# Optimization experiments

Measured on AMD Instinct MI355X. Metric: run time of the kernel, lower is better.

Reference implementation:

```python
import jax, jax.numpy as jnp
import numpy as np

VOCAB_SIZE = 126
N_LABELS = VOCAB_SIZE + 2  # 128
START_IDX = N_LABELS - 2
STOP_IDX = N_LABELS - 1
NEG_INF = -10000.0


def setup_inputs() -> dict:
    key = jax.random.key(0)
    k1, k2, k3 = jax.random.split(key, 3)
    B, T = 512, 512
    logits = jax.random.normal(k1, (B, T, N_LABELS), dtype=jnp.float32)
    lens = jax.random.randint(k2, (B,), 1, T + 1, dtype=jnp.int64)
    transitions = jax.random.normal(k3, (N_LABELS, N_LABELS), dtype=jnp.float32)
    # CRF constraints from __init__: nothing transitions FROM start-as-target row,
    # nothing transitions INTO stop column (transitions[i, j] = score j -> i).
    transitions = transitions.at[START_IDX, :].set(NEG_INF)
    transitions = transitions.at[:, STOP_IDX].set(NEG_INF)
    return {"logits": logits, "lens": lens, "transitions": transitions}


def reference(logits, lens, transitions):
    """CRF forward algorithm (log partition function). Returns [B] norm."""
    B, T, n = logits.shape
    alpha0 = jnp.full((B, n), NEG_INF, dtype=logits.dtype).at[:, START_IDX].set(0.0)
    # mask[t, b] = 1 while t < lens[b] (matches c_lens > 0 per-step update)
    mask = (jnp.arange(T)[:, None] < lens[None, :]).astype(logits.dtype)  # [T, B]
    logits_t = jnp.transpose(logits, (1, 0, 2))  # [T, B, n]

    def step(alpha, inp):
        logit, m = inp  # [B, n], [B]
        # alpha_nxt[b, i] = logit[b, i] + logsumexp_j(trans[i, j] + alpha[b, j])
        alpha_nxt = jax.nn.logsumexp(transitions[None, :, :] + alpha[:, None, :], axis=2) + logit
        m = m[:, None]
        alpha = m * alpha_nxt + (1.0 - m) * alpha
        return alpha, None

    alpha, _ = jax.lax.scan(step, alpha0, (logits_t, mask))
    alpha = alpha + transitions[STOP_IDX][None, :]
    return jax.nn.logsumexp(alpha, axis=1)  # [B]
```

## Files before the change

### kernel.cpp

```cpp
#include <hip/hip_runtime.h>

#define NL 128
#define TT 512
#define NB 512
#define START_IDX 126
#define STOP_IDX 127

typedef __attribute__((ext_vector_type(8))) short bf16x8;
typedef __attribute__((ext_vector_type(4))) float f32x4;

__device__ __forceinline__ short f2bf(float x) {
    union { float f; unsigned u; } v; v.f = x;
    unsigned r = (v.u + 0x7FFFu + ((v.u >> 16) & 1u)) >> 16;
    return (short)r;
}

__global__ __launch_bounds__(256, 2)
void crf_fwd_kernel(const float* __restrict__ logits,
                    const int* __restrict__ lens,
                    const float* __restrict__ trans,
                    float* __restrict__ out)
{
    const int b    = blockIdx.x;
    const int tid  = threadIdx.x;
    const int wave = tid >> 6;
    const int lane = tid & 63;
    const int col  = lane & 15;
    const int kgrp = lane >> 4;

    __shared__ __align__(16) short Vbuf[2][NL];
    __shared__ float red[4];

    bf16x8 bfrag[2][4];
    #pragma unroll
    for (int n = 0; n < 2; ++n) {
        const int label = wave * 32 + n * 16 + col;
        #pragma unroll
        for (int kk = 0; kk < 4; ++kk) {
            const float* tp = trans + label * NL + kk * 32 + kgrp * 8;
            bf16x8 f;
            #pragma unroll
            for (int m = 0; m < 8; ++m) f[m] = f2bf(__expf(tp[m]));
            bfrag[n][kk] = f;
        }
    }
    const int lbl0 = wave * 32 + col;
    const int lbl1 = lbl0 + 16;
    const float ets0 = __expf(trans[STOP_IDX * NL + lbl0]);
    const float ets1 = __expf(trans[STOP_IDX * NL + lbl1]);

    int len = lens[b];
    len = len < 1 ? 1 : (len > TT ? TT : len);

    if (tid < NL) Vbuf[0][tid] = (tid == START_IDX) ? (short)0x3F80 : (short)0;

    const float* lg = logits + (size_t)b * (TT * NL);
    float l0 = lg[lbl0];
    float l1 = lg[lbl1];
    float c  = 0.f;
    float nv0 = 0.f, nv1 = 0.f;

    __syncthreads();

    for (int t = 0; t < len; ++t) {
        const short* vb = Vbuf[t & 1];
        const int tn = (t + 1 < len) ? t + 1 : t;
        const float pl0 = lg[tn * NL + lbl0];
        const float pl1 = lg[tn * NL + lbl1];

        f32x4 acc0 = {0.f, 0.f, 0.f, 0.f};
        f32x4 acc1 = {0.f, 0.f, 0.f, 0.f};
        #pragma unroll
        for (int kk = 0; kk < 4; ++kk) {
            bf16x8 af = *(const bf16x8*)(vb + kk * 32 + kgrp * 8);
            acc0 = __builtin_amdgcn_mfma_f32_16x16x32_bf16(af, bfrag[0][kk], acc0, 0, 0, 0);
            acc1 = __builtin_amdgcn_mfma_f32_16x16x32_bf16(af, bfrag[1][kk], acc1, 0, 0, 0);
        }

        nv0 = acc0[0] * __expf(l0);
        nv1 = acc1[0] * __expf(l1);

        if ((t & 3) == 3) {
            float m = fmaxf(nv0, nv1);
            m = fmaxf(m, __shfl_xor(m, 1));
            m = fmaxf(m, __shfl_xor(m, 2));
            m = fmaxf(m, __shfl_xor(m, 4));
            m = fmaxf(m, __shfl_xor(m, 8));
            if (lane == 0) red[wave] = m;
            __syncthreads();
            m = fmaxf(fmaxf(red[0], red[1]), fmaxf(red[2], red[3]));
            union { float f; unsigned u; } mu; mu.f = m;
            const int eb = (int)(mu.u >> 23);
            union { float f; unsigned u; } sc;
            sc.u = (unsigned)(253 - eb) << 23;
            nv0 *= sc.f; nv1 *= sc.f;
            c += (float)(eb - 126) * 0.69314718055994531f;
        }

        if (lane < 16) {
            short* vw = Vbuf[(t + 1) & 1];
            vw[lbl0] = f2bf(nv0);
            vw[lbl1] = f2bf(nv1);
        }
        l0 = pl0; l1 = pl1;
        __syncthreads();
    }

    float p = nv0 * ets0 + nv1 * ets1;
    p += __shfl_xor(p, 1);
    p += __shfl_xor(p, 2);
    p += __shfl_xor(p, 4);
    p += __shfl_xor(p, 8);
    if (lane == 0) red[wave] = p;
    __syncthreads();
    if (tid == 0) out[b] = c + __logf(red[0] + red[1] + red[2] + red[3]);
}

extern "C" void kernel_launch(void* const* d_in, const int* in_sizes, int n_in,
                              void* d_out, int out_size, void* d_ws, size_t ws_size,
                              hipStream_t stream) {
    const float* logits = (const float*)d_in[0];
    const int*   lens   = (const int*)d_in[1];
    const float* trans  = (const float*)d_in[2];
    float*       outp   = (float*)d_out;
    crf_fwd_kernel<<<NB, 256, 0, stream>>>(logits, lens, trans, outp);
}
```

Measured before the change: 187.7 us.

## Batch 16 sequences per wave with register-resident alpha and exp precompute

Replaces the one-block-per-sequence scan with a single-wave kernel that handles 16 sequences at once. The transposed problem puts exp(transitions) in MFMA A fragments and keeps alpha packed as bf16 in registers, so the per-step LDS round trip and block barriers go away. A separate pre-pass writes exp(logits) into workspace in a permuted order, with a fallback that computes exp inline. Renormalisation now runs every 8 steps, and logits are prefetched two steps ahead. The catch is that only 32 waves are launched, which leaves most of the GPU idle, and each wave iterates to the longest length among its 16 sequences.

```diff
diff --git a/kernel.cpp b/kernel.cpp
--- a/kernel.cpp
+++ b/kernel.cpp
@@ -8,6 +8,7 @@
 
 typedef __attribute__((ext_vector_type(8))) short bf16x8;
 typedef __attribute__((ext_vector_type(4))) float f32x4;
+typedef __attribute__((ext_vector_type(4))) unsigned u32x4;
 
 __device__ __forceinline__ short f2bf(float x) {
     union { float f; unsigned u; } v; v.f = x;
@@ -15,105 +16,165 @@
     return (short)r;
 }
 
-__global__ __launch_bounds__(256, 2)
-void crf_fwd_kernel(const float* __restrict__ logits,
-                    const int* __restrict__ lens,
-                    const float* __restrict__ trans,
-                    float* __restrict__ out)
+__device__ __forceinline__ unsigned cvt_pk_bf16(float lo, float hi) {
+    unsigned r;
+    asm("v_cvt_pk_bf16_f32 %0, %1, %2" : "=v"(r) : "v"(lo), "v"(hi));
+    return r;
+}
+
+__global__ __launch_bounds__(256)
+void exp_pre(const float* __restrict__ logits, const int* __restrict__ lens,
+             float* __restrict__ elp)
 {
-    const int b    = blockIdx.x;
-    const int tid  = threadIdx.x;
-    const int wave = tid >> 6;
-    const int lane = tid & 63;
-    const int col  = lane & 15;
-    const int kgrp = lane >> 4;
+    const int b = blockIdx.x;
+    int len = lens[b]; len = len < 1 ? 1 : (len > TT ? TT : len);
+    const float* src = logits + (size_t)b * TT * NL;
+    float*       dst = elp    + (size_t)b * TT * NL;
+    for (int idx = threadIdx.x; idx < len * 32; idx += 256) {
+        const int t = idx >> 5, q = idx & 31;
+        const int lbl = (q & 7) * 16 + (q >> 3) * 4;
+        f32x4 v = *(const f32x4*)(src + t * NL + lbl);
+        f32x4 e = { __expf(v[0]), __expf(v[1]), __expf(v[2]), __expf(v[3]) };
+        *(f32x4*)(dst + t * NL + q * 4) = e;
+    }
+}
 
-    __shared__ __align__(16) short Vbuf[2][NL];
-    __shared__ float red[4];
+#define LOADEL(E, T_) do {                                                    \
+    const float* _p = elsrc + lbase + (size_t)(T_) * NL;                      \
+    _Pragma("unroll")                                                         \
+    for (int m_ = 0; m_ < 8; ++m_) {                                          \
+        const int off_ = RAW ? (m_ * 16 + 4 * g) : (g * 32 + m_ * 4);         \
+        E[m_] = *(const f32x4*)(_p + off_);                                   \
+    }                                                                         \
+} while (0)
 
-    bf16x8 bfrag[2][4];
+#define STEP(T_, ECUR) do {                                                   \
+    f32x4 acc_[8];                                                            \
+    _Pragma("unroll") for (int m_ = 0; m_ < 8; ++m_)                          \
+        acc_[m_] = (f32x4){0.f, 0.f, 0.f, 0.f};                               \
+    _Pragma("unroll") for (int kk_ = 0; kk_ < 4; ++kk_) {                     \
+        u32x4 bu_ = { bw[kk_][0], bw[kk_][1], bw[kk_][2], bw[kk_][3] };       \
+        bf16x8 bv_ = __builtin_bit_cast(bf16x8, bu_);                         \
+        _Pragma("unroll") for (int m_ = 0; m_ < 8; ++m_)                      \
+            acc_[m_] = __builtin_amdgcn_mfma_f32_16x16x32_bf16(               \
+                afr[m_][kk_], bv_, acc_[m_], 0, 0, 0);                        \
+    }                                                                         \
+    const bool live_ = (T_) < len;                                            \
+    float nv_[8][4];                                                          \
+    _Pragma("unroll") for (int m_ = 0; m_ < 8; ++m_)                          \
+        _Pragma("unroll") for (int r_ = 0; r_ < 4; ++r_) {                    \
+            float el_ = ECUR[m_][r_];                                         \
+            if (RAW) el_ = __expf(el_);                                       \
+            nv_[m_][r_] = acc_[m_][r_] * el_;                                 \
+        }                                                                     \
+    { int tl_ = (T_) + 2; if (tl_ > TT - 1) tl_ = TT - 1; LOADEL(ECUR, tl_); }\
+    if ((((T_) & 7) == 7)) {                                                  \
+        float mx_ = nv_[0][0];                                                \
+        _Pragma("unroll") for (int m_ = 0; m_ < 8; ++m_)                      \
+            _Pragma("unroll") for (int r_ = 0; r_ < 4; ++r_)                  \
+                mx_ = fmaxf(mx_, nv_[m_][r_]);                                \
+        mx_ = fmaxf(mx_, __shfl_xor(mx_, 16));                                \
+        mx_ = fmaxf(mx_, __shfl_xor(mx_, 32));                                \
+        const unsigned eb_ = (__float_as_uint(mx_) >> 23) & 0xFFu;            \
+        const float sc_ = __uint_as_float(((253u - eb_) & 0xFFu) << 23);      \
+        _Pragma("unroll") for (int m_ = 0; m_ < 8; ++m_)                      \
+            _Pragma("unroll") for (int r_ = 0; r_ < 4; ++r_)                  \
+                nv_[m_][r_] *= sc_;                                           \
+        if (live_) cb += (float)((int)eb_ - 126) * 0.69314718055994531f;      \
+    }                                                                         \
+    _Pragma("unroll") for (int kk_ = 0; kk_ < 4; ++kk_) {                     \
+        const unsigned p0_ = cvt_pk_bf16(nv_[kk_][0],     nv_[kk_][1]);       \
+        const unsigned p1_ = cvt_pk_bf16(nv_[kk_][2],     nv_[kk_][3]);       \
+        const unsigned p2_ = cvt_pk_bf16(nv_[kk_ + 4][0], nv_[kk_ + 4][1]);   \
+        const unsigned p3_ = cvt_pk_bf16(nv_[kk_ + 4][2], nv_[kk_ + 4][3]);   \
+        if (live_) {                                                          \
+            bw[kk_][0] = p0_; bw[kk_][1] = p1_;                               \
+            bw[kk_][2] = p2_; bw[kk_][3] = p3_;                               \
+        }                                                                     \
+    }                                                                         \
+} while (0)
+
+template<bool RAW>
+__global__ __launch_bounds__(64)
+void crf_scan(const float* __restrict__ logits,
+              const int* __restrict__ lens,
+              const float* __restrict__ trans,
+              const float* __restrict__ elp,
+              float* __restrict__ out)
+{
+    const int b0   = blockIdx.x * 16;
+    const int lane = threadIdx.x;
+    const int c    = lane & 15;
+    const int g    = lane >> 4;
+
+    bf16x8 afr[8][4];
     #pragma unroll
-    for (int n = 0; n < 2; ++n) {
-        const int label = wave * 32 + n * 16 + col;
+    for (int m = 0; m < 8; ++m) {
+        const float* rowp = trans + (m * 16 + c) * NL + 4 * g;
         #pragma unroll
         for (int kk = 0; kk < 4; ++kk) {
-            const float* tp = trans + label * NL + kk * 32 + kgrp * 8;
-            bf16x8 f;
+            f32x4 lo4 = *(const f32x4*)(rowp + kk * 16);
+            f32x4 hi4 = *(const f32x4*)(rowp + (kk + 4) * 16);
+            bf16x8 a;
             #pragma unroll
-            for (int m = 0; m < 8; ++m) f[m] = f2bf(__expf(tp[m]));
-            bfrag[n][kk] = f;
+            for (int j = 0; j < 4; ++j) {
+                a[j]     = f2bf(__expf(lo4[j]));
+                a[j + 4] = f2bf(__expf(hi4[j]));
+            }
+            afr[m][kk] = a;
         }
     }
-    const int lbl0 = wave * 32 + col;
-    const int lbl1 = lbl0 + 16;
-    const float ets0 = __expf(trans[STOP_IDX * NL + lbl0]);
-    const float ets1 = __expf(trans[STOP_IDX * NL + lbl1]);
 
-    int len = lens[b];
-    len = len < 1 ? 1 : (len > TT ? TT : len);
-
-    if (tid < NL) Vbuf[0][tid] = (tid == START_IDX) ? (short)0x3F80 : (short)0;
-
-    const float* lg = logits + (size_t)b * (TT * NL);
-    float l0 = lg[lbl0];
-    float l1 = lg[lbl1];
-    float c  = 0.f;
-    float nv0 = 0.f, nv1 = 0.f;
-
-    __syncthreads();
-
-    for (int t = 0; t < len; ++t) {
-        const short* vb = Vbuf[t & 1];
-        const int tn = (t + 1 < len) ? t + 1 : t;
-        const float pl0 = lg[tn * NL + lbl0];
-        const float pl1 = lg[tn * NL + lbl1];
-
-        f32x4 acc0 = {0.f, 0.f, 0.f, 0.f};
-        f32x4 acc1 = {0.f, 0.f, 0.f, 0.f};
-        #pragma unroll
-        for (int kk = 0; kk < 4; ++kk) {
-            bf16x8 af = *(const bf16x8*)(vb + kk * 32 + kgrp * 8);
-            acc0 = __builtin_amdgcn_mfma_f32_16x16x32_bf16(af, bfrag[0][kk], acc0, 0, 0, 0);
-            acc1 = __builtin_amdgcn_mfma_f32_16x16x32_bf16(af, bfrag[1][kk], acc1, 0, 0, 0);
-        }
-
-        nv0 = acc0[0] * __expf(l0);
-        nv1 = acc1[0] * __expf(l1);
-
-        if ((t & 3) == 3) {
-            float m = fmaxf(nv0, nv1);
-            m = fmaxf(m, __shfl_xor(m, 1));
-            m = fmaxf(m, __shfl_xor(m, 2));
-            m = fmaxf(m, __shfl_xor(m, 4));
-            m = fmaxf(m, __shfl_xor(m, 8));
-            if (lane == 0) red[wave] = m;
-            __syncthreads();
-            m = fmaxf(fmaxf(red[0], red[1]), fmaxf(red[2], red[3]));
-            union { float f; unsigned u; } mu; mu.f = m;
-            const int eb = (int)(mu.u >> 23);
-            union { float f; unsigned u; } sc;
-            sc.u = (unsigned)(253 - eb) << 23;
-            nv0 *= sc.f; nv1 *= sc.f;
-            c += (float)(eb - 126) * 0.69314718055994531f;
-        }
-
-        if (lane < 16) {
-            short* vw = Vbuf[(t + 1) & 1];
-            vw[lbl0] = f2bf(nv0);
-            vw[lbl1] = f2bf(nv1);
-        }
-        l0 = pl0; l1 = pl1;
-        __syncthreads();
+    int len = lens[b0 + c]; len = len < 1 ? 1 : (len > TT ? TT : len);
+    int glen = len;
+    #pragma unroll
+    for (int d = 1; d < 16; d <<= 1) {
+        int o = __shfl_xor(glen, d);
+        glen = glen > o ? glen : o;
     }
 
-    float p = nv0 * ets0 + nv1 * ets1;
-    p += __shfl_xor(p, 1);
-    p += __shfl_xor(p, 2);
-    p += __shfl_xor(p, 4);
-    p += __shfl_xor(p, 8);
-    if (lane == 0) red[wave] = p;
-    __syncthreads();
-    if (tid == 0) out[b] = c + __logf(red[0] + red[1] + red[2] + red[3]);
+    unsigned bw[4][4];
+    #pragma unroll
+    for (int kk = 0; kk < 4; ++kk)
+        #pragma unroll
+        for (int i = 0; i < 4; ++i) bw[kk][i] = 0u;
+    if (g == 3) bw[3][3] = 0x00003F80u;
+
+    float cb = 0.f;
+    const size_t lbase = (size_t)(b0 + c) * TT * NL;
+    const float* elsrc = RAW ? logits : elp;
+
+    f32x4 e0[8], e1[8];
+    LOADEL(e0, 0);
+    LOADEL(e1, 1);
+
+    for (int t = 0; t < glen; t += 2) {
+        STEP(t,     e0);
+        STEP(t + 1, e1);
+    }
+
+    float s = 0.f;
+    const float* stopr = trans + STOP_IDX * NL + 4 * g;
+    #pragma unroll
+    for (int kk = 0; kk < 4; ++kk) {
+        f32x4 t0 = *(const f32x4*)(stopr + kk * 16);
+        f32x4 t1 = *(const f32x4*)(stopr + (kk + 4) * 16);
+        #pragma unroll
+        for (int i = 0; i < 2; ++i) {
+            const unsigned w = bw[kk][i];
+            s += __uint_as_float(w << 16)          * __expf(t0[2 * i]);
+            s += __uint_as_float(w & 0xFFFF0000u)  * __expf(t0[2 * i + 1]);
+        }
+        #pragma unroll
+        for (int i = 2; i < 4; ++i) {
+            const unsigned w = bw[kk][i];
+            s += __uint_as_float(w << 16)          * __expf(t1[2 * (i - 2)]);
+            s += __uint_as_float(w & 0xFFFF0000u)  * __expf(t1[2 * (i - 2) + 1]);
+        }
+    }
+    s += __shfl_xor(s, 16);
+    s += __shfl_xor(s, 32);
+    if (lane < 16) out[b0 + c] = cb + __logf(s);
 }
 
 extern "C" void kernel_launch(void* const* d_in, const int* in_sizes, int n_in,
@@ -123,5 +184,13 @@
     const int*   lens   = (const int*)d_in[1];
     const float* trans  = (const float*)d_in[2];
     float*       outp   = (float*)d_out;
-    crf_fwd_kernel<<<NB, 256, 0, stream>>>(logits, lens, trans, outp);
+
+    const size_t need = (size_t)NB * TT * NL * sizeof(float);
+    if (ws_size >= need) {
+        float* elp = (float*)d_ws;
+        exp_pre<<<NB, 256, 0, stream>>>(logits, lens, elp);
+        crf_scan<false><<<NB / 16, 64, 0, stream>>>(logits, lens, trans, elp, outp);
+    } else {
+        crf_scan<true><<<NB / 16, 64, 0, stream>>>(logits, lens, trans, nullptr, outp);
+    }
 }
```

Measured after the change: 349.6 us. +86.2%, slower.
